# Kernel optimization log

Hardware: AMD Instinct MI355X
Metric: run time of the kernel (lower is better)

Reference implementation:

```python
import jax, jax.numpy as jnp
import numpy as np

N = 100000   # nodes
E = 1600000  # edges
IN = 128     # in_node_channels
H = 128      # hidden_channels
EPS = 1e-5   # BatchNorm eps


def _gcn_conv(x, W, b, src, dst, n):
    # x' = W x, then symmetric-normalized aggregation with self-loops (PyG GCNConv)
    xw = x @ W                                             # [N, H]
    loop = jnp.arange(n, dtype=src.dtype)
    src_f = jnp.concatenate([src, loop])                   # [E+N]
    dst_f = jnp.concatenate([dst, loop])
    deg = jax.ops.segment_sum(jnp.ones(src_f.shape, xw.dtype), dst_f, num_segments=n)
    dis = jax.lax.rsqrt(jnp.maximum(deg, 1.0))             # deg >= 1 due to self-loops
    norm = dis[src_f] * dis[dst_f]                         # [E+N]
    msg = xw[src_f] * norm[:, None]                        # gather + scale
    out = jax.ops.segment_sum(msg, dst_f, num_segments=n)  # scatter-add
    return out + b


def _bn(x, gamma, beta):
    # training-mode BatchNorm1d over the node dimension
    m = jnp.mean(x, axis=0)
    v = jnp.mean(jnp.square(x - m), axis=0)
    return gamma * (x - m) * jax.lax.rsqrt(v + EPS) + beta


def setup_inputs() -> dict:
    key = jax.random.key(0)
    ks = jax.random.split(key, 8)
    glorot = lambda k, shape, fan: jax.random.normal(k, shape, jnp.float32) / np.sqrt(fan).astype(np.float32)
    x = jax.random.normal(ks[0], (N, IN), jnp.float32)
    edge_index = jax.random.randint(ks[1], (2, E), 0, N, dtype=jnp.int32)
    return {
        "x": x,
        "edge_index": edge_index,
        "W1": glorot(ks[2], (IN, H), IN), "b1": jnp.zeros((H,), jnp.float32),
        "g1": jnp.ones((H,), jnp.float32), "be1": jnp.zeros((H,), jnp.float32),
        "W2": glorot(ks[3], (H, H), H), "b2": jnp.zeros((H,), jnp.float32),
        "g2": jnp.ones((H,), jnp.float32), "be2": jnp.zeros((H,), jnp.float32),
        "Wm1": glorot(ks[4], (H, 64), H), "bm1": jnp.zeros((64,), jnp.float32),
        "Wm2": glorot(ks[5], (64, 1), 64), "bm2": jnp.zeros((1,), jnp.float32),
    }


def reference(x, edge_index, W1, b1, g1, be1, W2, b2, g2, be2, Wm1, bm1, Wm2, bm2):
    src, dst = edge_index[0], edge_index[1]
    h = jax.nn.relu(_bn(_gcn_conv(x, W1, b1, src, dst, N), g1, be1))
    h = jax.nn.relu(_bn(_gcn_conv(h, W2, b2, src, dst, N), g2, be2))
    # MLP head (dropout is identity in eval / deterministic reference)
    h = jax.nn.relu(h @ Wm1 + bm1)
    out = h @ Wm2 + bm2                                     # [N, 1]
    return jnp.squeeze(out, axis=-1)                        # [N]
```

## Files before the change

kernel.cpp:

```cpp
#include <hip/hip_runtime.h>
#include <hip/hip_fp16.h>

#define HC 128
#define EPS_BN 1e-5f
#define NSTRIPE 8
#define AGG_BLOCKS 3072
#define BSHIFT 9
#define BNODES (1 << BSHIFT)
#define BCAP 12288
#define CHUNK 8192
#define SRC_BITS 18

typedef _Float16 f16;
typedef f16  f16x8 __attribute__((ext_vector_type(8)));
typedef float f32x4 __attribute__((ext_vector_type(4)));

struct GemmSmem {
    f16 Ah[128][136];
    f16 Bh[128][136];
    float sc[HC], sh[HC];
};

template<int SRC_F16, int TRANS, int SCALE, int SELFW>
__device__ __forceinline__ void gemm_body(GemmSmem& sm, int row0,
        const void* __restrict__ Xv, const f16* __restrict__ Wt,
        const float* __restrict__ W32, const float* __restrict__ stats,
        const float* __restrict__ gamma, const float* __restrict__ beta,
        const float* __restrict__ dis, f16* __restrict__ Y, int n) {
    const int tid = threadIdx.x;

    if constexpr (TRANS) {
        if (tid < 128) {
            float s = 0.f, q = 0.f;
#pragma unroll
            for (int t = 0; t < NSTRIPE; ++t) {
                s += stats[t * 256 + tid];
                q += stats[t * 256 + 128 + tid];
            }
            float m = s / (float)n;
            float v = q / (float)n - m * m;
            float scv = gamma[tid] * rsqrtf(fmaxf(v, 0.f) + EPS_BN);
            sm.sc[tid] = scv;
            sm.sh[tid] = beta[tid] - m * scv;
        }
    }

    if constexpr (SELFW) {
#pragma unroll
        for (int i = 0; i < 4; ++i) {
            int idx = i * 512 + tid;
            int g = idx >> 7, r = idx & 127;
#pragma unroll
            for (int j = 0; j < 8; ++j)
                sm.Bh[r][g * 8 + j] = (f16)W32[(size_t)(g * 8 + j) * HC + r];
        }
    } else {
#pragma unroll
        for (int i = 0; i < 4; ++i) {
            int idx = i * 512 + tid;
            int r = idx >> 4, g = idx & 15;
            *(f16x8*)&sm.Bh[r][g * 8] = *(const f16x8*)(Wt + (size_t)r * HC + g * 8);
        }
    }
    __syncthreads();

#pragma unroll
    for (int i = 0; i < 4; ++i) {
        int idx = i * 512 + tid;
        int r = idx >> 4, g = idx & 15;
        int grow = row0 + r;
        f16x8 h = {};
        if (grow < n) {
            if constexpr (SRC_F16) {
                f16x8 v = *(const f16x8*)((const f16*)Xv + (size_t)grow * HC + g * 8);
                if constexpr (TRANS) {
#pragma unroll
                    for (int j = 0; j < 8; ++j) {
                        float f = (float)v[j];
                        f = fmaxf(fmaf(f, sm.sc[g * 8 + j], sm.sh[g * 8 + j]), 0.f);
                        h[j] = (f16)f;
                    }
                } else h = v;
            } else {
                const float* X = (const float*)Xv;
                float4 a = *(const float4*)(X + (size_t)grow * HC + g * 8);
                float4 c = *(const float4*)(X + (size_t)grow * HC + g * 8 + 4);
                h[0] = (f16)a.x; h[1] = (f16)a.y; h[2] = (f16)a.z; h[3] = (f16)a.w;
                h[4] = (f16)c.x; h[5] = (f16)c.y; h[6] = (f16)c.z; h[7] = (f16)c.w;
            }
        }
        *(f16x8*)&sm.Ah[r][g * 8] = h;
    }
    __syncthreads();

    const int wv   = tid >> 6;
    const int lane = tid & 63;
    const int m    = lane & 15;
    const int kq   = (lane >> 4) * 8;

    f32x4 acc[8] = {};
#pragma unroll
    for (int kc = 0; kc < HC; kc += 32) {
        f16x8 a = *(const f16x8*)&sm.Ah[wv * 16 + m][kc + kq];
#pragma unroll
        for (int t = 0; t < 8; ++t) {
            f16x8 b = *(const f16x8*)&sm.Bh[t * 16 + m][kc + kq];
            acc[t] = __builtin_amdgcn_mfma_f32_16x16x32_f16(a, b, acc[t], 0, 0, 0);
        }
    }

    __syncthreads();
    {
        const int rg = (lane >> 4) * 4;
        float dv[4];
#pragma unroll
        for (int r = 0; r < 4; ++r) {
            if constexpr (SCALE) {
                int grow = row0 + wv * 16 + rg + r;
                dv[r] = (grow < n) ? dis[grow] : 0.f;
            } else dv[r] = 1.f;
        }
#pragma unroll
        for (int t = 0; t < 8; ++t)
#pragma unroll
            for (int r = 0; r < 4; ++r)
                sm.Ah[wv * 16 + rg + r][t * 16 + m] = (f16)(acc[t][r] * dv[r]);
    }
    __syncthreads();
#pragma unroll
    for (int i = 0; i < 4; ++i) {
        int idx = i * 512 + tid;
        int r = idx >> 4, g = idx & 15;
        int grow = row0 + r;
        if (grow < n)
            *(f16x8*)(Y + (size_t)grow * HC + g * 8) = *(const f16x8*)&sm.Ah[r][g * 8];
    }
}

__global__ __launch_bounds__(512) void fused_bin_gemm(
        const int* __restrict__ src, const int* __restrict__ dst,
        int* __restrict__ gcur, unsigned int* __restrict__ packed, int E,
        const float* __restrict__ x, const float* __restrict__ W1,
        f16* __restrict__ xws, int n, int binBlocks, int gemmBlocks,
        const float* __restrict__ W2, const float* __restrict__ Wm1,
        f16* __restrict__ Wt2, f16* __restrict__ Wm1t) {
    __shared__ GemmSmem sm;
    const int bi = blockIdx.x;
    if (bi < binBlocks) {
        int* cnt = (int*)&sm;
        int* cur = cnt + 256;
        const int tid = threadIdx.x;
        if (bi == 0 && tid < HC) xws[(size_t)n * HC + tid] = (f16)0.f;
        const int e0 = bi * CHUNK;
        int dreg[16];
        if (tid < 256) cnt[tid] = 0;
        __syncthreads();
#pragma unroll
        for (int i = 0; i < 16; ++i) {
            int e = e0 + i * 512 + tid;
            dreg[i] = (e < E) ? dst[e] : -1;
            if (dreg[i] >= 0) atomicAdd(&cnt[dreg[i] >> BSHIFT], 1);
        }
        __syncthreads();
        if (tid < 256) cur[tid] = (cnt[tid] > 0) ? atomicAdd(&gcur[tid], cnt[tid]) : 0;
        __syncthreads();
#pragma unroll
        for (int i = 0; i < 16; ++i) {
            int e = e0 + i * 512 + tid;
            if (dreg[i] >= 0) {
                int s = src[e];
                int b = dreg[i] >> BSHIFT;
                int pos = b * BCAP + atomicAdd(&cur[b], 1);
                packed[pos] = ((unsigned)(dreg[i] & (BNODES - 1)) << SRC_BITS) | (unsigned)s;
            }
        }
    } else if (bi < binBlocks + gemmBlocks) {
        gemm_body<0, 0, 0, 1>(sm, (bi - binBlocks) * 128, x, nullptr, W1,
                              nullptr, nullptr, nullptr, nullptr, xws, n);
    } else {
        int idx = (bi - binBlocks - gemmBlocks) * 512 + threadIdx.x;
        if (idx < 16384) {
            int k = idx >> 7, c = idx & 127;
            Wt2[(size_t)c * HC + k] = (f16)W2[idx];
        } else if (idx < 24576) {
            int i = idx - 16384;
            int c = i >> 7, k = i & 127;
            Wm1t[(size_t)c * HC + k] = (f16)Wm1[(size_t)k * 64 + c];
        }
    }
}

__global__ __launch_bounds__(1024) void sort_scale(const unsigned int* __restrict__ packed,
                                                   const int* __restrict__ gcur,
                                                   int2* __restrict__ rowptr2,
                                                   float* __restrict__ dis,
                                                   int* __restrict__ srcs,
                                                   f16* __restrict__ xws, int n) {
    __shared__ int cnt[BNODES];
    __shared__ int cur[BNODES];
    __shared__ int scn[BNODES];
    __shared__ float dsc[BNODES];
    const int b = blockIdx.x;
    const int node0 = b << BSHIFT;
    const int tid = threadIdx.x;
    const int base = b * BCAP;
    const int end  = base + gcur[b];

    if (tid < BNODES) cnt[tid] = 0;
    __syncthreads();
    for (int e = base + tid; e < end; e += 1024)
        atomicAdd(&cnt[packed[e] >> SRC_BITS], 1);
    __syncthreads();
    if (tid < BNODES) {
        float dv = rsqrtf((float)cnt[tid] + 1.f);
        dsc[tid] = dv;
        int node = node0 + tid;
        if (node < n) dis[node] = dv;
        scn[tid] = cnt[tid];
    }
    __syncthreads();
    for (int idx = tid; idx < BNODES * 16; idx += 1024) {
        int r = idx >> 4, gg = idx & 15;
        int node = node0 + r;
        if (node < n) {
            f16x8* p = (f16x8*)(xws + (size_t)node * HC + gg * 8);
            f16x8 v = *p;
            float dv = dsc[r];
#pragma unroll
            for (int j = 0; j < 8; ++j) v[j] = (f16)((float)v[j] * dv);
            *p = v;
        }
    }
    for (int off = 1; off < BNODES; off <<= 1) {
        int t = 0;
        if (tid < BNODES && tid >= off) t = scn[tid - off];
        __syncthreads();
        if (tid < BNODES) scn[tid] += t;
        __syncthreads();
    }
    if (tid < BNODES) {
        int excl = scn[tid] - cnt[tid];
        int node = node0 + tid;
        if (node < n)
            rowptr2[node] = make_int2(base + excl, base + excl + cnt[tid]);
        cur[tid] = excl;
    }
    __syncthreads();
    for (int e = base + tid; e < end; e += 1024) {
        unsigned p = packed[e];
        int pos = atomicAdd(&cur[p >> SRC_BITS], 1);
        srcs[base + pos] = (int)(p & ((1u << SRC_BITS) - 1));
    }
}

__global__ __launch_bounds__(512) void gemm_k(const void* __restrict__ Xv,
                                              const f16* __restrict__ Wt,
                                              const float* __restrict__ stats,
                                              const float* __restrict__ gamma,
                                              const float* __restrict__ beta,
                                              const float* __restrict__ dis,
                                              f16* __restrict__ Y, int n) {
    __shared__ GemmSmem sm;
    gemm_body<1, 1, 1, 0>(sm, blockIdx.x * 128, Xv, Wt, nullptr,
                          stats, gamma, beta, dis, Y, n);
}

__global__ __launch_bounds__(256) void gcn_agg_f16(const f16* __restrict__ xws,
                                                   const int* __restrict__ srcs,
                                                   const int2* __restrict__ rowptr2,
                                                   const float* __restrict__ dis,
                                                   const float* __restrict__ bias,
                                                   f16* __restrict__ out,
                                                   float* __restrict__ stats,
                                                   int n, int nwaves) {
    __shared__ float lds_s[4][128], lds_q[4][128];
    const int wv   = threadIdx.x >> 6;
    const int lane = threadIdx.x & 63;
    const int g    = lane >> 4;
    const int cg   = lane & 15;

    float b8[8];
#pragma unroll
    for (int j = 0; j < 8; ++j) b8[j] = bias[cg * 8 + j];

    float s8[8] = {}, q8[8] = {};

    for (int node = blockIdx.x * 4 + wv; node < n; node += nwaves) {
        const int2 rp = rowptr2[node];
        const int e1 = rp.y;
        float acc[8] = {};
        int e  = rp.x;
        int i0 = e + g, i1 = i0 + 4, i2 = i0 + 8, i3 = i0 + 12;
        int s0 = (i0 < e1) ? srcs[i0] : n;
        int s1 = (i1 < e1) ? srcs[i1] : n;
        int s2 = (i2 < e1) ? srcs[i2] : n;
        int s3 = (i3 < e1) ? srcs[i3] : n;
        while (e < e1) {
            int en = e + 16;
            int j0 = en + g, j1 = j0 + 4, j2 = j0 + 8, j3 = j0 + 12;
            int t0 = (j0 < e1) ? srcs[j0] : n;
            int t1 = (j1 < e1) ? srcs[j1] : n;
            int t2 = (j2 < e1) ? srcs[j2] : n;
            int t3 = (j3 < e1) ? srcs[j3] : n;
            f16x8 v0 = *(const f16x8*)(xws + (size_t)s0 * HC + cg * 8);
            f16x8 v1 = *(const f16x8*)(xws + (size_t)s1 * HC + cg * 8);
            f16x8 v2 = *(const f16x8*)(xws + (size_t)s2 * HC + cg * 8);
            f16x8 v3 = *(const f16x8*)(xws + (size_t)s3 * HC + cg * 8);
            f16x8 p01 = v0 + v1;
            f16x8 p23 = v2 + v3;
#pragma unroll
            for (int j = 0; j < 8; ++j)
                acc[j] += (float)p01[j] + (float)p23[j];
            s0 = t0; s1 = t1; s2 = t2; s3 = t3; e = en;
        }
#pragma unroll
        for (int j = 0; j < 8; ++j) acc[j] += __shfl_xor(acc[j], 16);
#pragma unroll
        for (int j = 0; j < 8; ++j) acc[j] += __shfl_xor(acc[j], 32);

        if (g == 0) {
            float dv = dis[node];
            f16x8 self = *(const f16x8*)(xws + (size_t)node * HC + cg * 8);
            f16x8 o;
#pragma unroll
            for (int j = 0; j < 8; ++j) {
                float r = fmaf(acc[j] + (float)self[j], dv, b8[j]);
                o[j] = (f16)r;
                s8[j] += r;
                q8[j] += r * r;
            }
            *(f16x8*)(out + (size_t)node * HC + cg * 8) = o;
        }
    }

    if (g == 0) {
#pragma unroll
        for (int j = 0; j < 8; ++j) {
            lds_s[wv][cg * 8 + j] = s8[j];
            lds_q[wv][cg * 8 + j] = q8[j];
        }
    }
    __syncthreads();
    float* stripe = stats + (size_t)(blockIdx.x & (NSTRIPE - 1)) * 256;
    if (threadIdx.x < 128) {
        float s = lds_s[0][threadIdx.x] + lds_s[1][threadIdx.x] +
                  lds_s[2][threadIdx.x] + lds_s[3][threadIdx.x];
        float q = lds_q[0][threadIdx.x] + lds_q[1][threadIdx.x] +
                  lds_q[2][threadIdx.x] + lds_q[3][threadIdx.x];
        atomicAdd(&stripe[threadIdx.x], s);
        atomicAdd(&stripe[128 + threadIdx.x], q);
    }
}

__global__ __launch_bounds__(256) void mlp_mfma(const f16* __restrict__ h,
                                                const float* __restrict__ stats,
                                                const float* __restrict__ gamma,
                                                const float* __restrict__ beta,
                                                const f16* __restrict__ Wm1t,
                                                const float* __restrict__ bm1,
                                                const float* __restrict__ Wm2,
                                                const float* __restrict__ bm2,
                                                float* __restrict__ out, int n) {
    __shared__ f16 Hs[64][136];
    __shared__ f16 Ws[64][136];
    __shared__ float sc[HC], sh[HC], bmv[64], w2v[64];
    const int tid  = threadIdx.x;
    const int row0 = blockIdx.x * 64;

    if (tid < 128) {
        float s = 0.f, q = 0.f;
#pragma unroll
        for (int t = 0; t < NSTRIPE; ++t) {
            s += stats[t * 256 + tid];
            q += stats[t * 256 + 128 + tid];
        }
        float m = s / (float)n;
        float v = q / (float)n - m * m;
        float scv = gamma[tid] * rsqrtf(fmaxf(v, 0.f) + EPS_BN);
        sc[tid] = scv;
        sh[tid] = beta[tid] - m * scv;
    }
    if (tid < 64) { bmv[tid] = bm1[tid]; w2v[tid] = Wm2[tid]; }

#pragma unroll
    for (int i = 0; i < 4; ++i) {
        int idx = i * 256 + tid;
        int r = idx >> 4, g = idx & 15;
        *(f16x8*)&Ws[r][g * 8] = *(const f16x8*)(Wm1t + (size_t)r * HC + g * 8);
    }
    __syncthreads();

#pragma unroll
    for (int i = 0; i < 4; ++i) {
        int idx = i * 256 + tid;
        int r = idx >> 4, g = idx & 15;
        int grow = row0 + r;
        f16x8 hv = {};
        if (grow < n) {
            f16x8 v = *(const f16x8*)(h + (size_t)grow * HC + g * 8);
#pragma unroll
            for (int j = 0; j < 8; ++j) {
                float f = (float)v[j];
                f = fmaxf(fmaf(f, sc[g * 8 + j], sh[g * 8 + j]), 0.f);
                hv[j] = (f16)f;
            }
        }
        *(f16x8*)&Hs[r][g * 8] = hv;
    }
    __syncthreads();

    const int wv   = tid >> 6;
    const int lane = tid & 63;
    const int m    = lane & 15;
    const int kq   = (lane >> 4) * 8;

    f32x4 acc[4] = {};
#pragma unroll
    for (int kc = 0; kc < HC; kc += 32) {
        f16x8 a = *(const f16x8*)&Hs[wv * 16 + m][kc + kq];
#pragma unroll
        for (int t = 0; t < 4; ++t) {
            f16x8 b = *(const f16x8*)&Ws[t * 16 + m][kc + kq];
            acc[t] = __builtin_amdgcn_mfma_f32_16x16x32_f16(a, b, acc[t], 0, 0, 0);
        }
    }

    float part[4];
#pragma unroll
    for (int reg = 0; reg < 4; ++reg) {
        float s = 0.f;
#pragma unroll
        for (int t = 0; t < 4; ++t) {
            int col = t * 16 + m;
            s += fmaxf(acc[t][reg] + bmv[col], 0.f) * w2v[col];
        }
        part[reg] = s;
    }
#pragma unroll
    for (int off = 1; off < 16; off <<= 1) {
#pragma unroll
        for (int reg = 0; reg < 4; ++reg)
            part[reg] += __shfl_xor(part[reg], off);
    }
    if (m == 0) {
        int rbase = row0 + wv * 16 + (lane >> 4) * 4;
        float bb = bm2[0];
#pragma unroll
        for (int reg = 0; reg < 4; ++reg) {
            int row = rbase + reg;
            if (row < n) out[row] = part[reg] + bb;
        }
    }
}

extern "C" void kernel_launch(void* const* d_in, const int* in_sizes, int n_in,
                              void* d_out, int out_size, void* d_ws, size_t ws_size,
                              hipStream_t stream) {
    const float* x   = (const float*)d_in[0];
    const int*   ei  = (const int*)  d_in[1];
    const float* W1  = (const float*)d_in[2];
    const float* b1  = (const float*)d_in[3];
    const float* g1  = (const float*)d_in[4];
    const float* be1 = (const float*)d_in[5];
    const float* W2  = (const float*)d_in[6];
    const float* b2  = (const float*)d_in[7];
    const float* g2  = (const float*)d_in[8];
    const float* be2 = (const float*)d_in[9];
    const float* Wm1 = (const float*)d_in[10];
    const float* bm1 = (const float*)d_in[11];
    const float* Wm2 = (const float*)d_in[12];
    const float* bm2 = (const float*)d_in[13];
    float* out = (float*)d_out;

    const int n = in_sizes[0] / HC;
    const int E = in_sizes[1] / 2;
    const int* srcp = ei;
    const int* dstp = ei + E;
    const int nb = (n + BNODES - 1) >> BSHIFT;

    char* ws = (char*)d_ws;
    size_t off = 0;
    auto alloc = [&](size_t bytes) { void* p = ws + off; off = (off + bytes + 511) & ~511ULL; return p; };
    float*  dis     = (float*) alloc((size_t)n * 4);
    int2*   rowptr2 = (int2*)  alloc((size_t)n * 8);
    int*    gcur    = (int*)   alloc(1024);
    float*  stats   = (float*) alloc(2 * NSTRIPE * 256 * 4);
    float*  stats1  = stats;
    float*  stats2  = stats + NSTRIPE * 256;
    unsigned int* packed = (unsigned int*)alloc((size_t)nb * BCAP * 4);
    int*    srcs    = (int*)   alloc((size_t)nb * BCAP * 4);
    f16*    xws     = (f16*)   alloc((size_t)(n + 1) * HC * 2);
    f16*    bufBh   = (f16*)   alloc((size_t)n * HC * 2);
    f16*    Wt2     = (f16*)   alloc((size_t)HC * HC * 2);
    f16*    Wm1t    = (f16*)   alloc((size_t)64 * HC * 2);

    const int gemmBlocks = (n + 127) / 128;
    const int mlpBlocks  = (n + 63) / 64;
    const int binBlocks  = (E + CHUNK - 1) / CHUNK;
    const int wprepBlks  = 48;
    const int aggWaves   = AGG_BLOCKS * 4;

    hipMemsetAsync(gcur, 0, 1024 + 2 * NSTRIPE * 256 * 4, stream);

    fused_bin_gemm<<<binBlocks + gemmBlocks + wprepBlks, 512, 0, stream>>>(
        srcp, dstp, gcur, packed, E, x, W1, xws, n, binBlocks, gemmBlocks,
        W2, Wm1, Wt2, Wm1t);

    sort_scale<<<nb, 1024, 0, stream>>>(packed, gcur, rowptr2, dis, srcs, xws, n);

    gcn_agg_f16<<<AGG_BLOCKS, 256, 0, stream>>>(xws, srcs, rowptr2, dis, b1,
                                                bufBh, stats1, n, aggWaves);

    gemm_k<<<gemmBlocks, 512, 0, stream>>>(bufBh, Wt2, stats1, g1, be1,
                                           dis, xws, n);
    gcn_agg_f16<<<AGG_BLOCKS, 256, 0, stream>>>(xws, srcs, rowptr2, dis, b2,
                                                bufBh, stats2, n, aggWaves);

    mlp_mfma<<<mlpBlocks, 256, 0, stream>>>(bufBh, stats2, g2, be2, Wm1t, bm1, Wm2, bm2,
                                            out, n);
}
```

Before: 329.1 us.

## Compute degrees in a pre-pass and fold dis scaling into the first GEMM epilogue

Adds a kernel that counts in-degrees with global atomics and converts W1, W2 and Wm1 to transposed fp16 in the same launch. With degrees known before the first GEMM, that GEMM now applies the rsqrt(deg+1) row scale in its epilogue, and the sort kernel no longer re-reads and rewrites the whole xws matrix. This removes a full read-modify-write pass over N×128 fp16. The cost is an extra launch, E global atomics on deg, and rsqrt recomputed from deg in the aggregation and GEMM kernels.

New measurement: 393.4 us. 1.2x slower.

```diff
diff --git a/kernel.cpp b/kernel.cpp
--- a/kernel.cpp
+++ b/kernel.cpp
@@ -10,6 +10,7 @@
 #define BCAP 12288
 #define CHUNK 8192
 #define SRC_BITS 18
+#define DEGB 216
 
 typedef _Float16 f16;
 typedef f16  f16x8 __attribute__((ext_vector_type(8)));
@@ -21,12 +22,43 @@
     float sc[HC], sh[HC];
 };
 
-template<int SRC_F16, int TRANS, int SCALE, int SELFW>
+__global__ __launch_bounds__(1024) void deg_wprep(const int* __restrict__ dst,
+                                                  int* __restrict__ deg, int E,
+                                                  const float* __restrict__ W1,
+                                                  const float* __restrict__ W2,
+                                                  const float* __restrict__ Wm1,
+                                                  f16* __restrict__ Wt1,
+                                                  f16* __restrict__ Wt2,
+                                                  f16* __restrict__ Wm1t,
+                                                  int wprepBlks) {
+    const int tid = threadIdx.x;
+    if (blockIdx.x < (unsigned)wprepBlks) {
+        int idx = blockIdx.x * 1024 + tid;
+        if (idx < 16384) {
+            int k = idx >> 7, c = idx & 127;
+            Wt1[(size_t)c * HC + k] = (f16)W1[idx];
+        } else if (idx < 32768) {
+            int i = idx - 16384;
+            int k = i >> 7, c = i & 127;
+            Wt2[(size_t)c * HC + k] = (f16)W2[i];
+        } else if (idx < 40960) {
+            int i = idx - 32768;
+            int c = i >> 7, k = i & 127;
+            Wm1t[(size_t)c * HC + k] = (f16)Wm1[(size_t)k * 64 + c];
+        }
+        return;
+    }
+    const int stride = DEGB * 1024;
+    for (int i = (blockIdx.x - wprepBlks) * 1024 + tid; i < E; i += stride)
+        atomicAdd(&deg[dst[i]], 1);
+}
+
+template<int SRC_F16, int TRANS>
 __device__ __forceinline__ void gemm_body(GemmSmem& sm, int row0,
         const void* __restrict__ Xv, const f16* __restrict__ Wt,
-        const float* __restrict__ W32, const float* __restrict__ stats,
+        const float* __restrict__ stats,
         const float* __restrict__ gamma, const float* __restrict__ beta,
-        const float* __restrict__ dis, f16* __restrict__ Y, int n) {
+        const int* __restrict__ deg, f16* __restrict__ Y, int n) {
     const int tid = threadIdx.x;
 
     if constexpr (TRANS) {
@@ -45,22 +77,11 @@
         }
     }
 
-    if constexpr (SELFW) {
-#pragma unroll
-        for (int i = 0; i < 4; ++i) {
-            int idx = i * 512 + tid;
-            int g = idx >> 7, r = idx & 127;
-#pragma unroll
-            for (int j = 0; j < 8; ++j)
-                sm.Bh[r][g * 8 + j] = (f16)W32[(size_t)(g * 8 + j) * HC + r];
-        }
-    } else {
-#pragma unroll
-        for (int i = 0; i < 4; ++i) {
-            int idx = i * 512 + tid;
-            int r = idx >> 4, g = idx & 15;
-            *(f16x8*)&sm.Bh[r][g * 8] = *(const f16x8*)(Wt + (size_t)r * HC + g * 8);
-        }
+#pragma unroll
+    for (int i = 0; i < 4; ++i) {
+        int idx = i * 512 + tid;
+        int r = idx >> 4, g = idx & 15;
+        *(f16x8*)&sm.Bh[r][g * 8] = *(const f16x8*)(Wt + (size_t)r * HC + g * 8);
     }
     __syncthreads();
 
@@ -115,10 +136,8 @@
         float dv[4];
 #pragma unroll
         for (int r = 0; r < 4; ++r) {
-            if constexpr (SCALE) {
-                int grow = row0 + wv * 16 + rg + r;
-                dv[r] = (grow < n) ? dis[grow] : 0.f;
-            } else dv[r] = 1.f;
+            int grow = row0 + wv * 16 + rg + r;
+            dv[r] = (grow < n) ? rsqrtf((float)deg[grow] + 1.f) : 0.f;
         }
 #pragma unroll
         for (int t = 0; t < 8; ++t)
@@ -137,20 +156,18 @@
     }
 }
 
-__global__ __launch_bounds__(512) void fused_bin_gemm(
+__global__ __launch_bounds__(512) void fused_bin_gemm1(
         const int* __restrict__ src, const int* __restrict__ dst,
         int* __restrict__ gcur, unsigned int* __restrict__ packed, int E,
-        const float* __restrict__ x, const float* __restrict__ W1,
-        f16* __restrict__ xws, int n, int binBlocks, int gemmBlocks,
-        const float* __restrict__ W2, const float* __restrict__ Wm1,
-        f16* __restrict__ Wt2, f16* __restrict__ Wm1t) {
+        const float* __restrict__ x, const f16* __restrict__ Wt1,
+        const int* __restrict__ deg, f16* __restrict__ xws, int n,
+        int binBlocks) {
     __shared__ GemmSmem sm;
     const int bi = blockIdx.x;
     if (bi < binBlocks) {
         int* cnt = (int*)&sm;
         int* cur = cnt + 256;
         const int tid = threadIdx.x;
-        if (bi == 0 && tid < HC) xws[(size_t)n * HC + tid] = (f16)0.f;
         const int e0 = bi * CHUNK;
         int dreg[16];
         if (tid < 256) cnt[tid] = 0;
@@ -174,32 +191,19 @@
                 packed[pos] = ((unsigned)(dreg[i] & (BNODES - 1)) << SRC_BITS) | (unsigned)s;
             }
         }
-    } else if (bi < binBlocks + gemmBlocks) {
-        gemm_body<0, 0, 0, 1>(sm, (bi - binBlocks) * 128, x, nullptr, W1,
-                              nullptr, nullptr, nullptr, nullptr, xws, n);
     } else {
-        int idx = (bi - binBlocks - gemmBlocks) * 512 + threadIdx.x;
-        if (idx < 16384) {
-            int k = idx >> 7, c = idx & 127;
-            Wt2[(size_t)c * HC + k] = (f16)W2[idx];
-        } else if (idx < 24576) {
-            int i = idx - 16384;
-            int c = i >> 7, k = i & 127;
-            Wm1t[(size_t)c * HC + k] = (f16)Wm1[(size_t)k * 64 + c];
-        }
-    }
-}
-
-__global__ __launch_bounds__(1024) void sort_scale(const unsigned int* __restrict__ packed,
-                                                   const int* __restrict__ gcur,
-                                                   int2* __restrict__ rowptr2,
-                                                   float* __restrict__ dis,
-                                                   int* __restrict__ srcs,
-                                                   f16* __restrict__ xws, int n) {
+        gemm_body<0, 0>(sm, (bi - binBlocks) * 128, x, Wt1,
+                        nullptr, nullptr, nullptr, deg, xws, n);
+    }
+}
+
+__global__ __launch_bounds__(1024) void sort_k(const unsigned int* __restrict__ packed,
+                                               const int* __restrict__ gcur,
+                                               int2* __restrict__ rowptr2,
+                                               int* __restrict__ srcs, int n) {
     __shared__ int cnt[BNODES];
     __shared__ int cur[BNODES];
     __shared__ int scn[BNODES];
-    __shared__ float dsc[BNODES];
     const int b = blockIdx.x;
     const int node0 = b << BSHIFT;
     const int tid = threadIdx.x;
@@ -211,26 +215,8 @@
     for (int e = base + tid; e < end; e += 1024)
         atomicAdd(&cnt[packed[e] >> SRC_BITS], 1);
     __syncthreads();
-    if (tid < BNODES) {
-        float dv = rsqrtf((float)cnt[tid] + 1.f);
-        dsc[tid] = dv;
-        int node = node0 + tid;
-        if (node < n) dis[node] = dv;
-        scn[tid] = cnt[tid];
-    }
-    __syncthreads();
-    for (int idx = tid; idx < BNODES * 16; idx += 1024) {
-        int r = idx >> 4, gg = idx & 15;
-        int node = node0 + r;
-        if (node < n) {
-            f16x8* p = (f16x8*)(xws + (size_t)node * HC + gg * 8);
-            f16x8 v = *p;
-            float dv = dsc[r];
-#pragma unroll
-            for (int j = 0; j < 8; ++j) v[j] = (f16)((float)v[j] * dv);
-            *p = v;
-        }
-    }
+    if (tid < BNODES) scn[tid] = cnt[tid];
+    __syncthreads();
     for (int off = 1; off < BNODES; off <<= 1) {
         int t = 0;
         if (tid < BNODES && tid >= off) t = scn[tid - off];
@@ -258,17 +244,16 @@
                                               const float* __restrict__ stats,
                                               const float* __restrict__ gamma,
                                               const float* __restrict__ beta,
-                                              const float* __restrict__ dis,
+                                              const int* __restrict__ deg,
                                               f16* __restrict__ Y, int n) {
     __shared__ GemmSmem sm;
-    gemm_body<1, 1, 1, 0>(sm, blockIdx.x * 128, Xv, Wt, nullptr,
-                          stats, gamma, beta, dis, Y, n);
+    gemm_body<1, 1>(sm, blockIdx.x * 128, Xv, Wt, stats, gamma, beta, deg, Y, n);
 }
 
 __global__ __launch_bounds__(256) void gcn_agg_f16(const f16* __restrict__ xws,
                                                    const int* __restrict__ srcs,
                                                    const int2* __restrict__ rowptr2,
-                                                   const float* __restrict__ dis,
+                                                   const int* __restrict__ deg,
                                                    const float* __restrict__ bias,
                                                    f16* __restrict__ out,
                                                    float* __restrict__ stats,
@@ -319,7 +304,7 @@
         for (int j = 0; j < 8; ++j) acc[j] += __shfl_xor(acc[j], 32);
 
         if (g == 0) {
-            float dv = dis[node];
+            float dv = rsqrtf((float)deg[node] + 1.f);
             f16x8 self = *(const f16x8*)(xws + (size_t)node * HC + cg * 8);
             f16x8 o;
 #pragma unroll
@@ -481,39 +466,43 @@
     char* ws = (char*)d_ws;
     size_t off = 0;
     auto alloc = [&](size_t bytes) { void* p = ws + off; off = (off + bytes + 511) & ~511ULL; return p; };
-    float*  dis     = (float*) alloc((size_t)n * 4);
-    int2*   rowptr2 = (int2*)  alloc((size_t)n * 8);
     int*    gcur    = (int*)   alloc(1024);
     float*  stats   = (float*) alloc(2 * NSTRIPE * 256 * 4);
+    int*    deg     = (int*)   alloc((size_t)n * 4);
     float*  stats1  = stats;
     float*  stats2  = stats + NSTRIPE * 256;
+    int2*   rowptr2 = (int2*)  alloc((size_t)n * 8);
     unsigned int* packed = (unsigned int*)alloc((size_t)nb * BCAP * 4);
     int*    srcs    = (int*)   alloc((size_t)nb * BCAP * 4);
     f16*    xws     = (f16*)   alloc((size_t)(n + 1) * HC * 2);
     f16*    bufBh   = (f16*)   alloc((size_t)n * HC * 2);
+    f16*    Wt1     = (f16*)   alloc((size_t)HC * HC * 2);
     f16*    Wt2     = (f16*)   alloc((size_t)HC * HC * 2);
     f16*    Wm1t    = (f16*)   alloc((size_t)64 * HC * 2);
 
     const int gemmBlocks = (n + 127) / 128;
     const int mlpBlocks  = (n + 63) / 64;
     const int binBlocks  = (E + CHUNK - 1) / CHUNK;
-    const int wprepBlks  = 48;
+    const int wprepBlks  = 40;
     const int aggWaves   = AGG_BLOCKS * 4;
 
-    hipMemsetAsync(gcur, 0, 1024 + 2 * NSTRIPE * 256 * 4, stream);
-
-    fused_bin_gemm<<<binBlocks + gemmBlocks + wprepBlks, 512, 0, stream>>>(
-        srcp, dstp, gcur, packed, E, x, W1, xws, n, binBlocks, gemmBlocks,
-        W2, Wm1, Wt2, Wm1t);
-
-    sort_scale<<<nb, 1024, 0, stream>>>(packed, gcur, rowptr2, dis, srcs, xws, n);
-
-    gcn_agg_f16<<<AGG_BLOCKS, 256, 0, stream>>>(xws, srcs, rowptr2, dis, b1,
+    hipMemsetAsync(gcur, 0, 1024 + 2 * NSTRIPE * 256 * 4 + (size_t)n * 4, stream);
+    hipMemsetAsync(xws + (size_t)n * HC, 0, HC * 2, stream);
+
+    deg_wprep<<<wprepBlks + DEGB, 1024, 0, stream>>>(dstp, deg, E, W1, W2, Wm1,
+                                                     Wt1, Wt2, Wm1t, wprepBlks);
+
+    fused_bin_gemm1<<<binBlocks + gemmBlocks, 512, 0, stream>>>(
+        srcp, dstp, gcur, packed, E, x, Wt1, deg, xws, n, binBlocks);
+
+    sort_k<<<nb, 1024, 0, stream>>>(packed, gcur, rowptr2, srcs, n);
+
+    gcn_agg_f16<<<AGG_BLOCKS, 256, 0, stream>>>(xws, srcs, rowptr2, deg, b1,
                                                 bufBh, stats1, n, aggWaves);
 
     gemm_k<<<gemmBlocks, 512, 0, stream>>>(bufBh, Wt2, stats1, g1, be1,
-                                           dis, xws, n);
-    gcn_agg_f16<<<AGG_BLOCKS, 256, 0, stream>>>(xws, srcs, rowptr2, dis, b2,
+                                           deg, xws, n);
+    gcn_agg_f16<<<AGG_BLOCKS, 256, 0, stream>>>(xws, srcs, rowptr2, deg, b2,
                                                 bufBh, stats2, n, aggWaves);
 
     mlp_mfma<<<mlpBlocks, 256, 0, stream>>>(bufBh, stats2, g2, be2, Wm1t, bm1, Wm2, bm2,
```
